# Performance work log

Measured on AMD Instinct MI355X. Metric: run time of the kernel, lower is better.

The kernel has to match this reference:

```python
import jax, jax.numpy as jnp
import numpy as np

N_NODES = 100000
N_EDGES = 1600000
IN_F = 64
HIDDEN = 128
HIDDEN2 = HIDDEN // 2
N_CLASSES = 10


def setup_inputs() -> dict:
    key = jax.random.key(0)
    ks = jax.random.split(key, 8)
    x = jax.random.normal(ks[0], (N_NODES, IN_F), dtype=jnp.float32)
    edge_index = jax.random.randint(ks[1], (2, N_EDGES), 0, N_NODES, dtype=jnp.int64 if jax.config.jax_enable_x64 else jnp.int32)
    # Linear params (PyTorch nn.Linear: y = x @ W.T + b); store as [in, out] for einsum-free matmul
    def lin(k, fi, fo):
        bound = 1.0 / np.sqrt(fi)
        kw, kb = jax.random.split(k)
        W = jax.random.uniform(kw, (fi, fo), minval=-bound, maxval=bound, dtype=jnp.float32)
        b = jax.random.uniform(kb, (fo,), minval=-bound, maxval=bound, dtype=jnp.float32)
        return W, b
    W1, b1 = lin(ks[2], IN_F, HIDDEN)
    W2, b2 = lin(ks[3], HIDDEN, HIDDEN2)
    W3, b3 = lin(ks[4], HIDDEN2, N_CLASSES)
    return {"x": x, "edge_index": edge_index, "n_nodes": N_NODES,
            "W1": W1, "b1": b1, "W2": W2, "b2": b2, "W3": W3, "b3": b3}


def gcn_layer(x, row, col, n_nodes, W, b):
    # gather source features, scatter-add into destination nodes
    agg = jax.ops.segment_sum(x[row], col, num_segments=n_nodes)  # [N, F]
    deg = jax.ops.segment_sum(jnp.ones_like(col, dtype=x.dtype), col, num_segments=n_nodes)
    deg = jnp.maximum(deg, 1.0)
    return (agg / deg[:, None]) @ W + b


def reference(x, edge_index, n_nodes, W1, b1, W2, b2, W3, b3):
    row, col = edge_index[0], edge_index[1]
    h = jax.nn.relu(gcn_layer(x, row, col, n_nodes, W1, b1))
    # dropout is identity in eval mode
    h = jax.nn.relu(gcn_layer(h, row, col, n_nodes, W2, b2))
    return h @ W3 + b3
```

## Files before the change

### kernel.cpp

```cpp
#include <hip/hip_runtime.h>

#define N_NODES 100000
#define N_EDGES 1600000
#define IN_F 64
#define HID 128
#define HID2 64
#define NCLS 10

#define SEG 64

#define NBUCK 128
#define SUBR 782
#define CAP2 14000
#define EBA 6250

typedef __attribute__((ext_vector_type(8))) short bfrag;
typedef __attribute__((ext_vector_type(4))) float f32x4;

__device__ __forceinline__ unsigned short bf_rne(float f) {
  unsigned int u = __float_as_uint(f);
  u += 0x7fffu + ((u >> 16) & 1u);
  return (unsigned short)(u >> 16);
}

__global__ __launch_bounds__(256) void cast_k(const float* __restrict__ x,
                                              unsigned short* __restrict__ xb) {
  int i = blockIdx.x * blockDim.x + threadIdx.x;
  const float4* xf4 = (const float4*)x;
  float4 a = xf4[2 * i];
  float4 b = xf4[2 * i + 1];
  ushort4 o0, o1;
  o0.x = bf_rne(a.x); o0.y = bf_rne(a.y); o0.z = bf_rne(a.z); o0.w = bf_rne(a.w);
  o1.x = bf_rne(b.x); o1.y = bf_rne(b.y); o1.z = bf_rne(b.z); o1.w = bf_rne(b.w);
  ushort4* ob = (ushort4*)xb;
  ob[2 * i] = o0;
  ob[2 * i + 1] = o1;
}

__global__ __launch_bounds__(256) void wtrans_k(const float* __restrict__ W1,
                                                const float* __restrict__ W2,
                                                unsigned short* __restrict__ W1t,
                                                unsigned short* __restrict__ W2t) {
  int i = blockIdx.x * 256 + threadIdx.x;
  if (i < IN_F * HID) {
    int j = i >> 6, k = i & 63;
    W1t[i] = bf_rne(W1[k * HID + j]);
  } else {
    int i2 = i - IN_F * HID;
    int j = i2 >> 7, k = i2 & 127;
    W2t[i2] = bf_rne(W2[k * HID2 + j]);
  }
}

__global__ __launch_bounds__(256) void binA_k(const int* __restrict__ row,
                                              const int* __restrict__ col,
                                              int* __restrict__ bcnt,
                                              unsigned int* __restrict__ pairs) {
  __shared__ int hcnt[NBUCK];
  __shared__ int hbase[NBUCK];
  int t = threadIdx.x;
  if (t < NBUCK) hcnt[t] = 0;
  __syncthreads();
  int e0 = blockIdx.x * EBA;
  int e1 = e0 + EBA;
  for (int e = e0 + t; e < e1; e += 256) {
    int b = col[e] / SUBR;
    atomicAdd(&hcnt[b], 1);
  }
  __syncthreads();
  if (t < NBUCK) {
    hbase[t] = atomicAdd(&bcnt[t], hcnt[t]);
    hcnt[t] = 0;
  }
  __syncthreads();
  for (int e = e0 + t; e < e1; e += 256) {
    int dst = col[e];
    int src = row[e];
    int b = dst / SUBR;
    int pos = hbase[b] + atomicAdd(&hcnt[b], 1);
    pairs[(size_t)b * CAP2 + pos] =
        ((unsigned)(dst - b * SUBR) << 17) | (unsigned)src;
  }
}

__global__ __launch_bounds__(512) void binB_k(const unsigned int* __restrict__ pairs,
                                              const int* __restrict__ bcnt,
                                              int* __restrict__ cursors,
                                              int* __restrict__ csr_src) {
  __shared__ int cur[SUBR];
  int b = blockIdx.x;
  int t = threadIdx.x;
  int lo = b * SUBR;
  for (int i = t; i < SUBR; i += 512) cur[i] = 0;
  __syncthreads();
  int cnt = bcnt[b];
  const unsigned int* bp = pairs + (size_t)b * CAP2;
  for (int i = t; i < cnt; i += 512) {
    unsigned w = bp[i];
    int local = w >> 17;
    int src = (int)(w & 0x1ffffu);
    int pos = atomicAdd(&cur[local], 1);
    if (pos < SEG) csr_src[(size_t)(lo + local) * SEG + pos] = src;
  }
  __syncthreads();
  for (int i = t; i < SUBR; i += 512) {
    int n = lo + i;
    if (n < N_NODES) {
      int d = cur[i];
      if (d > SEG) d = SEG;
      cursors[n] = n * SEG + d;
      int cons = d <= 32 ? 32 : ((d + 15) & ~15);
      for (int q = d; q < cons; q++) csr_src[(size_t)n * SEG + q] = 0;
    }
  }
}

#define ACC1(r)                                                     \
  {                                                                 \
    ax += __uint_as_float((r).x << 16);                             \
    ay += __uint_as_float((r).x & 0xffff0000u);                     \
    az += __uint_as_float((r).y << 16);                             \
    aw += __uint_as_float((r).y & 0xffff0000u);                     \
  }
#define LD8(r, ia, ib)                                              \
  {                                                                 \
    r[0] = vb[(size_t)(unsigned)(ia).x * 16 + fc];                  \
    r[1] = vb[(size_t)(unsigned)(ia).y * 16 + fc];                  \
    r[2] = vb[(size_t)(unsigned)(ia).z * 16 + fc];                  \
    r[3] = vb[(size_t)(unsigned)(ia).w * 16 + fc];                  \
    r[4] = vb[(size_t)(unsigned)(ib).x * 16 + fc];                  \
    r[5] = vb[(size_t)(unsigned)(ib).y * 16 + fc];                  \
    r[6] = vb[(size_t)(unsigned)(ib).z * 16 + fc];                  \
    r[7] = vb[(size_t)(unsigned)(ib).w * 16 + fc];                  \
  }
#define NODE_BODY(i, rbuf, dd, EXTRA)                               \
  {                                                                 \
    float ax = 0.f, ay = 0.f, az = 0.f, aw = 0.f;                   \
    ACC1(rbuf[0]) ACC1(rbuf[1]) ACC1(rbuf[2]) ACC1(rbuf[3])         \
    ACC1(rbuf[4]) ACC1(rbuf[5]) ACC1(rbuf[6]) ACC1(rbuf[7])         \
    int cons = 32;                                                  \
    if (dd > 32) {                                                  \
      cons = (dd + 15) & ~15;                                       \
      int sbase = (n0 + i) * SEG;                                   \
      for (int p = sbase + 32; p < sbase + cons; p += 16) {         \
        int4 iT = csr4[(p >> 2) + eg];                              \
        uint2 t0 = vb[(size_t)(unsigned)iT.x * 16 + fc];            \
        uint2 t1 = vb[(size_t)(unsigned)iT.y * 16 + fc];            \
        uint2 t2 = vb[(size_t)(unsigned)iT.z * 16 + fc];            \
        uint2 t3 = vb[(size_t)(unsigned)iT.w * 16 + fc];            \
        ACC1(t0) ACC1(t1) ACC1(t2) ACC1(t3)                         \
      }                                                             \
    }                                                               \
    EXTRA                                                           \
    ax += __shfl_xor(ax, 16); ay += __shfl_xor(ay, 16);             \
    az += __shfl_xor(az, 16); aw += __shfl_xor(aw, 16);             \
    ax += __shfl_xor(ax, 32); ay += __shfl_xor(ay, 32);             \
    az += __shfl_xor(az, 32); aw += __shfl_xor(aw, 32);             \
    float pc = (float)(cons - dd);                                  \
    res[i] = make_float4(ax - pc * zx, ay - pc * zy,                \
                         az - pc * zz, aw - pc * zw);               \
    inv[i] = 1.0f / (dd < 1 ? 1.0f : (float)(dd));                  \
  }

__device__ __forceinline__ void gather4_bf16(
    const uint2* __restrict__ vb, const int* __restrict__ csr,
    const int* __restrict__ cursors, int n0, int eg, int fc,
    float4 res[4], float inv[4]) {
  const int4* csr4 = (const int4*)csr;
  size_t rb = (size_t)n0 * 16;
  int4 iA0 = csr4[rb + eg],      iB0 = csr4[rb + 4 + eg];
  int4 iA1 = csr4[rb + 16 + eg], iB1 = csr4[rb + 20 + eg];
  int4 iA2 = csr4[rb + 32 + eg], iB2 = csr4[rb + 36 + eg];
  int4 iA3 = csr4[rb + 48 + eg], iB3 = csr4[rb + 52 + eg];
  int d0 = cursors[n0 + 0] - (n0 + 0) * SEG;
  int d1 = cursors[n0 + 1] - (n0 + 1) * SEG;
  int d2 = cursors[n0 + 2] - (n0 + 2) * SEG;
  int d3 = cursors[n0 + 3] - (n0 + 3) * SEG;
  uint2 rA[8], rB[8], rC[8];
  LD8(rA, iA0, iB0)
  LD8(rB, iA1, iB1)
  LD8(rC, iA2, iB2)
  uint2 z = vb[fc];
  float zx = __uint_as_float(z.x << 16);
  float zy = __uint_as_float(z.x & 0xffff0000u);
  float zz = __uint_as_float(z.y << 16);
  float zw = __uint_as_float(z.y & 0xffff0000u);
  NODE_BODY(0, rA, d0, LD8(rA, iA3, iB3))
  NODE_BODY(1, rB, d1, )
  NODE_BODY(2, rC, d2, )
  NODE_BODY(3, rA, d3, )
}

#define NB1 32
#define XS_S 72
#define HS_S 136
#define W1_S 72
#define W2_S 136
__global__ __launch_bounds__(512, 4) void gmm1_k(
    const unsigned short* __restrict__ xb, const int* __restrict__ cursors,
    const int* __restrict__ csr_src, const unsigned short* __restrict__ W1t,
    const float* __restrict__ b1, const unsigned short* __restrict__ W2t,
    unsigned short* __restrict__ g) {
  __shared__ unsigned short W1l[HID * W1_S];
  __shared__ unsigned short W2l[HID2 * W2_S];
  __shared__ unsigned short xsb[NB1 * XS_S];
  __shared__ unsigned short hsb[NB1 * HS_S];
  __shared__ float b1l[HID];
  int t = threadIdx.x;
  {
    const uint2* s1 = (const uint2*)W1t;
    for (int i = t; i < HID * IN_F / 4; i += 512) {
      int j = i >> 4, k4 = i & 15;
      *(uint2*)&W1l[j * W1_S + k4 * 4] = s1[i];
    }
    const uint2* s2 = (const uint2*)W2t;
    for (int i = t; i < HID2 * HID / 4; i += 512) {
      int j = i >> 5, k4 = i & 31;
      *(uint2*)&W2l[j * W2_S + k4 * 4] = s2[i];
    }
    if (t < HID) b1l[t] = b1[t];
  }
  int node0 = blockIdx.x * NB1;
  int wave = t >> 6;
  int lane = t & 63;
  int eg = lane >> 4;
  int fc = lane & 15;
  {
    const uint2* vb = (const uint2*)xb;
    float4 res[4];
    float inv[4];
    gather4_bf16(vb, csr_src, cursors, node0 + wave * 4, eg, fc, res, inv);
    if (eg == 0) {
#pragma unroll
      for (int i = 0; i < 4; i++) {
        ushort4 o;
        o.x = bf_rne(res[i].x * inv[i]); o.y = bf_rne(res[i].y * inv[i]);
        o.z = bf_rne(res[i].z * inv[i]); o.w = bf_rne(res[i].w * inv[i]);
        *(ushort4*)&xsb[(wave * 4 + i) * XS_S + fc * 4] = o;
      }
    }
  }
  __syncthreads();
  int lr = lane & 15;
  int kb = lane >> 4;
  {
    int c = wave;
#pragma unroll
    for (int m = 0; m < 2; m++) {
      f32x4 acc = {0.f, 0.f, 0.f, 0.f};
#pragma unroll
      for (int s = 0; s < 2; s++) {
        bfrag af = *(const bfrag*)&xsb[(m * 16 + lr) * XS_S + s * 32 + kb * 8];
        bfrag bf = *(const bfrag*)&W1l[(c * 16 + lr) * W1_S + s * 32 + kb * 8];
        acc = __builtin_amdgcn_mfma_f32_16x16x32_bf16(af, bf, acc, 0, 0, 0);
      }
      int col = c * 16 + lr;
      float bb = b1l[col];
#pragma unroll
      for (int q = 0; q < 4; q++) {
        int r = m * 16 + kb * 4 + q;
        float v = acc[q] + bb;
        hsb[r * HS_S + col] = bf_rne(v > 0.0f ? v : 0.0f);
      }
    }
  }
  __syncthreads();
  {
    int m = wave >> 2, c = wave & 3;
    f32x4 acc = {0.f, 0.f, 0.f, 0.f};
#pragma unroll
    for (int s = 0; s < 4; s++) {
      bfrag af = *(const bfrag*)&hsb[(m * 16 + lr) * HS_S + s * 32 + kb * 8];
      bfrag bf = *(const bfrag*)&W2l[(c * 16 + lr) * W2_S + s * 32 + kb * 8];
      acc = __builtin_amdgcn_mfma_f32_16x16x32_bf16(af, bf, acc, 0, 0, 0);
    }
    int col = c * 16 + lr;
#pragma unroll
    for (int q = 0; q < 4; q++) {
      int r = m * 16 + kb * 4 + q;
      g[(size_t)(node0 + r) * HID2 + col] = bf_rne(acc[q]);
    }
  }
}

#define NBH 32
__global__ __launch_bounds__(512, 4) void ghead_k(
    const unsigned short* __restrict__ g, const int* __restrict__ cursors,
    const int* __restrict__ csr_src, const float* __restrict__ b2,
    const float* __restrict__ W3, const float* __restrict__ b3,
    float* __restrict__ out) {
  __shared__ float W3l[HID2 * NCLS];
  __shared__ float hs[NBH][HID2 + 4];
  int t = threadIdx.x;
  for (int i = t; i < HID2 * NCLS; i += 512) W3l[i] = W3[i];
  int node0 = blockIdx.x * NBH;
  int lane = t & 63;
  int wave = t >> 6;
  int eg = lane >> 4;
  int fc = lane & 15;
  {
    const uint2* vb = (const uint2*)g;
    const float4* b2f4 = (const float4*)b2;
    float4 res[4];
    float inv[4];
    gather4_bf16(vb, csr_src, cursors, node0 + wave * 4, eg, fc, res, inv);
    if (eg == 0) {
      float4 bb = b2f4[fc];
#pragma unroll
      for (int i = 0; i < 4; i++) {
        float4 v;
        v.x = res[i].x * inv[i] + bb.x; v.y = res[i].y * inv[i] + bb.y;
        v.z = res[i].z * inv[i] + bb.z; v.w = res[i].w * inv[i] + bb.w;
        v.x = v.x > 0.0f ? v.x : 0.0f;
        v.y = v.y > 0.0f ? v.y : 0.0f;
        v.z = v.z > 0.0f ? v.z : 0.0f;
        v.w = v.w > 0.0f ? v.w : 0.0f;
        *(float4*)&hs[wave * 4 + i][fc * 4] = v;
      }
    }
  }
  __syncthreads();
  if (t < NBH * NCLS) {
    int n = t / NCLS;
    int c = t - n * NCLS;
    float a = b3[c];
    for (int k = 0; k < HID2; k++) a += hs[n][k] * W3l[k * NCLS + c];
    out[(size_t)(node0 + n) * NCLS + c] = a;
  }
}

extern "C" void kernel_launch(void* const* d_in, const int* in_sizes, int n_in,
                              void* d_out, int out_size, void* d_ws, size_t ws_size,
                              hipStream_t stream) {
  const float* x  = (const float*)d_in[0];
  const int*   ei = (const int*)d_in[1];
  const int*   row = ei;
  const int*   col = ei + N_EDGES;
  const float* W1 = (const float*)d_in[3];
  const float* b1 = (const float*)d_in[4];
  const float* W2 = (const float*)d_in[5];
  const float* b2 = (const float*)d_in[6];
  const float* W3 = (const float*)d_in[7];
  const float* b3 = (const float*)d_in[8];
  float* out = (float*)d_out;

  char* ws = (char*)d_ws;
  int*            cursors = (int*)ws;
  int*            bcnt    = (int*)(ws + (512 << 10));
  unsigned short* W1t     = (unsigned short*)(ws + (520 << 10));
  unsigned short* W2t     = (unsigned short*)(ws + (552 << 10));
  int*            csr_src = (int*)(ws + (1 << 20));
  unsigned int*   pairs   = (unsigned int*)(ws + (28 << 20));
  unsigned short* xb      = (unsigned short*)(ws + (36 << 20));
  unsigned short* g       = (unsigned short*)(ws + (49 << 20));

  hipMemsetAsync(bcnt, 0, NBUCK * sizeof(int), stream);
  wtrans_k<<<(IN_F * HID + HID * HID2) / 256, 256, 0, stream>>>(W1, W2, W1t, W2t);
  cast_k<<<N_NODES * IN_F / 8 / 256, 256, 0, stream>>>(x, xb);
  binA_k<<<N_EDGES / EBA, 256, 0, stream>>>(row, col, bcnt, pairs);
  binB_k<<<NBUCK, 512, 0, stream>>>(pairs, bcnt, cursors, csr_src);

  gmm1_k<<<N_NODES / NB1, 512, 0, stream>>>(xb, cursors, csr_src, W1t, b1, W2t, g);

  ghead_k<<<N_NODES / NBH, 512, 0, stream>>>(g, cursors, csr_src, b2, W3, b3, out);
}
```

Baseline: 148.3 us.

## Drop LDS weight staging, shrink gather register footprint, rebucket edge binning finer

The GEMM kernel no longer stages W1/W2/b1 in shared memory. MFMA weight fragments are read straight from global memory (through cache), which cuts LDS use and lets launch bounds request 8 blocks per CU instead of 4. The gather helper now keeps two rolling index/feature buffers instead of three and hands results to a lambda callback, lowering register pressure for the higher occupancy. Edge binning moves to 256 buckets of 391 nodes with smaller edge chunks per block, giving more binA blocks and more binB blocks. The risk is repeated global weight loads per block and less memory-level parallelism in the gather.

```diff
diff --git a/kernel.cpp b/kernel.cpp
--- a/kernel.cpp
+++ b/kernel.cpp
@@ -9,10 +9,10 @@
 
 #define SEG 64
 
-#define NBUCK 128
-#define SUBR 782
-#define CAP2 14000
-#define EBA 6250
+#define NBUCK 256
+#define SUBR 391
+#define CAP2 7000
+#define EBA 1600
 
 typedef __attribute__((ext_vector_type(8))) short bfrag;
 typedef __attribute__((ext_vector_type(4))) float f32x4;
@@ -59,7 +59,7 @@
   __shared__ int hcnt[NBUCK];
   __shared__ int hbase[NBUCK];
   int t = threadIdx.x;
-  if (t < NBUCK) hcnt[t] = 0;
+  hcnt[t] = 0;
   __syncthreads();
   int e0 = blockIdx.x * EBA;
   int e1 = e0 + EBA;
@@ -68,10 +68,8 @@
     atomicAdd(&hcnt[b], 1);
   }
   __syncthreads();
-  if (t < NBUCK) {
-    hbase[t] = atomicAdd(&bcnt[t], hcnt[t]);
-    hcnt[t] = 0;
-  }
+  hbase[t] = atomicAdd(&bcnt[t], hcnt[t]);
+  hcnt[t] = 0;
   __syncthreads();
   for (int e = e0 + t; e < e1; e += 256) {
     int dst = col[e];
@@ -133,7 +131,7 @@
     r[6] = vb[(size_t)(unsigned)(ib).z * 16 + fc];                  \
     r[7] = vb[(size_t)(unsigned)(ib).w * 16 + fc];                  \
   }
-#define NODE_BODY(i, rbuf, dd, EXTRA)                               \
+#define NODE_BODY(i, rbuf, dd, ...)                                 \
   {                                                                 \
     float ax = 0.f, ay = 0.f, az = 0.f, aw = 0.f;                   \
     ACC1(rbuf[0]) ACC1(rbuf[1]) ACC1(rbuf[2]) ACC1(rbuf[3])         \
@@ -151,75 +149,63 @@
         ACC1(t0) ACC1(t1) ACC1(t2) ACC1(t3)                         \
       }                                                             \
     }                                                               \
-    EXTRA                                                           \
+    __VA_ARGS__                                                     \
     ax += __shfl_xor(ax, 16); ay += __shfl_xor(ay, 16);             \
     az += __shfl_xor(az, 16); aw += __shfl_xor(aw, 16);             \
     ax += __shfl_xor(ax, 32); ay += __shfl_xor(ay, 32);             \
     az += __shfl_xor(az, 32); aw += __shfl_xor(aw, 32);             \
     float pc = (float)(cons - dd);                                  \
-    res[i] = make_float4(ax - pc * zx, ay - pc * zy,                \
-                         az - pc * zz, aw - pc * zw);               \
-    inv[i] = 1.0f / (dd < 1 ? 1.0f : (float)(dd));                  \
-  }
-
+    emit(i, make_float4(ax - pc * zx, ay - pc * zy,                 \
+                        az - pc * zz, aw - pc * zw), dd);           \
+  }
+
+template <class F>
 __device__ __forceinline__ void gather4_bf16(
     const uint2* __restrict__ vb, const int* __restrict__ csr,
-    const int* __restrict__ cursors, int n0, int eg, int fc,
-    float4 res[4], float inv[4]) {
+    const int* __restrict__ cursors, int n0, int eg, int fc, F&& emit) {
   const int4* csr4 = (const int4*)csr;
   size_t rb = (size_t)n0 * 16;
-  int4 iA0 = csr4[rb + eg],      iB0 = csr4[rb + 4 + eg];
-  int4 iA1 = csr4[rb + 16 + eg], iB1 = csr4[rb + 20 + eg];
-  int4 iA2 = csr4[rb + 32 + eg], iB2 = csr4[rb + 36 + eg];
-  int4 iA3 = csr4[rb + 48 + eg], iB3 = csr4[rb + 52 + eg];
+  int4 iA0 = csr4[rb + eg];
+  int4 iB0 = csr4[rb + 4 + eg];
+  int4 iA1 = csr4[rb + 16 + eg];
+  int4 iB1 = csr4[rb + 20 + eg];
+  uint2 rA[8], rB[8];
+  LD8(rA, iA0, iB0)
+  LD8(rB, iA1, iB1)
   int d0 = cursors[n0 + 0] - (n0 + 0) * SEG;
   int d1 = cursors[n0 + 1] - (n0 + 1) * SEG;
   int d2 = cursors[n0 + 2] - (n0 + 2) * SEG;
   int d3 = cursors[n0 + 3] - (n0 + 3) * SEG;
-  uint2 rA[8], rB[8], rC[8];
-  LD8(rA, iA0, iB0)
-  LD8(rB, iA1, iB1)
-  LD8(rC, iA2, iB2)
   uint2 z = vb[fc];
   float zx = __uint_as_float(z.x << 16);
   float zy = __uint_as_float(z.x & 0xffff0000u);
   float zz = __uint_as_float(z.y << 16);
   float zw = __uint_as_float(z.y & 0xffff0000u);
-  NODE_BODY(0, rA, d0, LD8(rA, iA3, iB3))
-  NODE_BODY(1, rB, d1, )
-  NODE_BODY(2, rC, d2, )
-  NODE_BODY(3, rA, d3, )
+  NODE_BODY(0, rA, d0,
+    int4 iA2 = csr4[rb + 32 + eg];
+    int4 iB2 = csr4[rb + 36 + eg];
+    LD8(rA, iA2, iB2)
+  )
+  NODE_BODY(1, rB, d1,
+    int4 iA3 = csr4[rb + 48 + eg];
+    int4 iB3 = csr4[rb + 52 + eg];
+    LD8(rB, iA3, iB3)
+  )
+  NODE_BODY(2, rA, d2, )
+  NODE_BODY(3, rB, d3, )
 }
 
 #define NB1 32
 #define XS_S 72
 #define HS_S 136
-#define W1_S 72
-#define W2_S 136
-__global__ __launch_bounds__(512, 4) void gmm1_k(
+__global__ __launch_bounds__(512, 8) void gmm1_k(
     const unsigned short* __restrict__ xb, const int* __restrict__ cursors,
     const int* __restrict__ csr_src, const unsigned short* __restrict__ W1t,
     const float* __restrict__ b1, const unsigned short* __restrict__ W2t,
     unsigned short* __restrict__ g) {
-  __shared__ unsigned short W1l[HID * W1_S];
-  __shared__ unsigned short W2l[HID2 * W2_S];
   __shared__ unsigned short xsb[NB1 * XS_S];
   __shared__ unsigned short hsb[NB1 * HS_S];
-  __shared__ float b1l[HID];
   int t = threadIdx.x;
-  {
-    const uint2* s1 = (const uint2*)W1t;
-    for (int i = t; i < HID * IN_F / 4; i += 512) {
-      int j = i >> 4, k4 = i & 15;
-      *(uint2*)&W1l[j * W1_S + k4 * 4] = s1[i];
-    }
-    const uint2* s2 = (const uint2*)W2t;
-    for (int i = t; i < HID2 * HID / 4; i += 512) {
-      int j = i >> 5, k4 = i & 31;
-      *(uint2*)&W2l[j * W2_S + k4 * 4] = s2[i];
-    }
-    if (t < HID) b1l[t] = b1[t];
-  }
   int node0 = blockIdx.x * NB1;
   int wave = t >> 6;
   int lane = t & 63;
@@ -227,35 +213,32 @@
   int fc = lane & 15;
   {
     const uint2* vb = (const uint2*)xb;
-    float4 res[4];
-    float inv[4];
-    gather4_bf16(vb, csr_src, cursors, node0 + wave * 4, eg, fc, res, inv);
-    if (eg == 0) {
-#pragma unroll
-      for (int i = 0; i < 4; i++) {
-        ushort4 o;
-        o.x = bf_rne(res[i].x * inv[i]); o.y = bf_rne(res[i].y * inv[i]);
-        o.z = bf_rne(res[i].z * inv[i]); o.w = bf_rne(res[i].w * inv[i]);
-        *(ushort4*)&xsb[(wave * 4 + i) * XS_S + fc * 4] = o;
-      }
-    }
+    gather4_bf16(vb, csr_src, cursors, node0 + wave * 4, eg, fc,
+                 [&](int i, float4 a, int dd) {
+                   if (eg == 0) {
+                     float inv = 1.0f / (dd < 1 ? 1.0f : (float)dd);
+                     ushort4 o;
+                     o.x = bf_rne(a.x * inv); o.y = bf_rne(a.y * inv);
+                     o.z = bf_rne(a.z * inv); o.w = bf_rne(a.w * inv);
+                     *(ushort4*)&xsb[(wave * 4 + i) * XS_S + fc * 4] = o;
+                   }
+                 });
   }
   __syncthreads();
   int lr = lane & 15;
   int kb = lane >> 4;
   {
-    int c = wave;
+    int col = wave * 16 + lr;
+    bfrag wf0 = *(const bfrag*)&W1t[col * IN_F + kb * 8];
+    bfrag wf1 = *(const bfrag*)&W1t[col * IN_F + 32 + kb * 8];
+    float bb = b1[col];
 #pragma unroll
     for (int m = 0; m < 2; m++) {
       f32x4 acc = {0.f, 0.f, 0.f, 0.f};
-#pragma unroll
-      for (int s = 0; s < 2; s++) {
-        bfrag af = *(const bfrag*)&xsb[(m * 16 + lr) * XS_S + s * 32 + kb * 8];
-        bfrag bf = *(const bfrag*)&W1l[(c * 16 + lr) * W1_S + s * 32 + kb * 8];
-        acc = __builtin_amdgcn_mfma_f32_16x16x32_bf16(af, bf, acc, 0, 0, 0);
-      }
-      int col = c * 16 + lr;
-      float bb = b1l[col];
+      bfrag a0 = *(const bfrag*)&xsb[(m * 16 + lr) * XS_S + kb * 8];
+      bfrag a1 = *(const bfrag*)&xsb[(m * 16 + lr) * XS_S + 32 + kb * 8];
+      acc = __builtin_amdgcn_mfma_f32_16x16x32_bf16(a0, wf0, acc, 0, 0, 0);
+      acc = __builtin_amdgcn_mfma_f32_16x16x32_bf16(a1, wf1, acc, 0, 0, 0);
 #pragma unroll
       for (int q = 0; q < 4; q++) {
         int r = m * 16 + kb * 4 + q;
@@ -266,15 +249,15 @@
   }
   __syncthreads();
   {
-    int m = wave >> 2, c = wave & 3;
+    int m = wave >> 2;
+    int col = (wave & 3) * 16 + lr;
     f32x4 acc = {0.f, 0.f, 0.f, 0.f};
 #pragma unroll
     for (int s = 0; s < 4; s++) {
       bfrag af = *(const bfrag*)&hsb[(m * 16 + lr) * HS_S + s * 32 + kb * 8];
-      bfrag bf = *(const bfrag*)&W2l[(c * 16 + lr) * W2_S + s * 32 + kb * 8];
+      bfrag bf = *(const bfrag*)&W2t[col * HID + s * 32 + kb * 8];
       acc = __builtin_amdgcn_mfma_f32_16x16x32_bf16(af, bf, acc, 0, 0, 0);
     }
-    int col = c * 16 + lr;
 #pragma unroll
     for (int q = 0; q < 4; q++) {
       int r = m * 16 + kb * 4 + q;
@@ -284,7 +267,7 @@
 }
 
 #define NBH 32
-__global__ __launch_bounds__(512, 4) void ghead_k(
+__global__ __launch_bounds__(512, 8) void ghead_k(
     const unsigned short* __restrict__ g, const int* __restrict__ cursors,
     const int* __restrict__ csr_src, const float* __restrict__ b2,
     const float* __restrict__ W3, const float* __restrict__ b3,
@@ -301,23 +284,21 @@
   {
     const uint2* vb = (const uint2*)g;
     const float4* b2f4 = (const float4*)b2;
-    float4 res[4];
-    float inv[4];
-    gather4_bf16(vb, csr_src, cursors, node0 + wave * 4, eg, fc, res, inv);
-    if (eg == 0) {
-      float4 bb = b2f4[fc];
-#pragma unroll
-      for (int i = 0; i < 4; i++) {
-        float4 v;
-        v.x = res[i].x * inv[i] + bb.x; v.y = res[i].y * inv[i] + bb.y;
-        v.z = res[i].z * inv[i] + bb.z; v.w = res[i].w * inv[i] + bb.w;
-        v.x = v.x > 0.0f ? v.x : 0.0f;
-        v.y = v.y > 0.0f ? v.y : 0.0f;
-        v.z = v.z > 0.0f ? v.z : 0.0f;
-        v.w = v.w > 0.0f ? v.w : 0.0f;
-        *(float4*)&hs[wave * 4 + i][fc * 4] = v;
-      }
-    }
+    float4 bb = b2f4[fc];
+    gather4_bf16(vb, csr_src, cursors, node0 + wave * 4, eg, fc,
+                 [&](int i, float4 a, int dd) {
+                   if (eg == 0) {
+                     float inv = 1.0f / (dd < 1 ? 1.0f : (float)dd);
+                     float4 v;
+                     v.x = a.x * inv + bb.x; v.y = a.y * inv + bb.y;
+                     v.z = a.z * inv + bb.z; v.w = a.w * inv + bb.w;
+                     v.x = v.x > 0.0f ? v.x : 0.0f;
+                     v.y = v.y > 0.0f ? v.y : 0.0f;
+                     v.z = v.z > 0.0f ? v.z : 0.0f;
+                     v.w = v.w > 0.0f ? v.w : 0.0f;
+                     *(float4*)&hs[wave * 4 + i][fc * 4] = v;
+                   }
+                 });
   }
   __syncthreads();
   if (t < NBH * NCLS) {
@@ -354,7 +335,7 @@
   unsigned short* xb      = (unsigned short*)(ws + (36 << 20));
   unsigned short* g       = (unsigned short*)(ws + (49 << 20));
 
-  hipMemsetAsync(bcnt, 0, NBUCK * sizeof(int), stream);
+  (void)hipMemsetAsync(bcnt, 0, NBUCK * sizeof(int), stream);
   wtrans_k<<<(IN_F * HID + HID * HID2) / 256, 256, 0, stream>>>(W1, W2, W1t, W2t);
   cast_k<<<N_NODES * IN_F / 8 / 256, 256, 0, stream>>>(x, xb);
   binA_k<<<N_EDGES / EBA, 256, 0, stream>>>(row, col, bcnt, pairs);
```

New measurement: 228.1 us. 1.54x slower.
